# Kernel tuning notes

Measured on AMD Instinct MI355X. Metric: run time of the kernel, lower is better.

The kernel has to match this reference:

```python
import jax, jax.numpy as jnp
import numpy as np

C_IN, C_OUT = 256, 128

def setup_inputs() -> dict:
    key = jax.random.key(0)
    k1, k2, k3, k4, k5, k6 = jax.random.split(key, 6)
    B, H, W = 8, 64, 64
    p = jax.random.normal(k1, (B, C_IN, H, W), dtype=jnp.float32)
    b = jax.random.normal(k2, (B, C_IN, H, W), dtype=jnp.float32)
    # 1x1 conv weights (Conv2d with kernel 1 == pointwise matmul) + biases
    sq = 1.0 / np.sqrt(C_IN)
    Wq = jax.random.uniform(k3, (C_OUT, C_IN), jnp.float32, -sq, sq)
    bq = jax.random.uniform(k4, (C_OUT,), jnp.float32, -sq, sq)
    Wk = jax.random.uniform(k5, (C_OUT, C_IN), jnp.float32, -sq, sq)
    bk = jax.random.uniform(k6, (C_OUT,), jnp.float32, -sq, sq)
    return {"p": p, "b": b, "Wq": Wq, "bq": bq, "Wk": Wk, "bk": bk}

def reference(p, b, Wq, bq, Wk, bk):
    B, C, H, W = p.shape
    N = H * W
    # 1x1 convs -> flatten spatial dim to N
    q = jnp.einsum('bchw,oc->bhwo', p, Wq) + bq          # [B,H,W,Co]
    q = q.reshape(B, N, -1).astype(jnp.float32)           # [B,N,Co] (query permuted)
    k = jnp.einsum('bchw,oc->bohw', b, Wk) + bk[None, :, None, None]
    k = k.reshape(B, -1, N).astype(jnp.float32)           # [B,Co,N]
    energy = jnp.einsum('bnc,bcm->bnm', q, k)             # [B,N,N] unscaled
    attention = jax.nn.softmax(energy, axis=-1)           # softmax over keys
    value = b.reshape(B, C, N)                            # [B,C,N]
    out = jnp.einsum('bnm,bcm->bcn', attention, value)    # [B,C,N]
    return out.reshape(B, C, H, W)
```

## Files before the change

### kernel.cpp

```cpp
#include <hip/hip_runtime.h>
#include <hip/hip_bf16.h>
#include <math.h>


#define B_   8
#define CIN  256
#define COUT 128
#define NN   4096

typedef _Float16 half8  __attribute__((ext_vector_type(8)));
typedef short    short8 __attribute__((ext_vector_type(8)));
typedef float    f32x4  __attribute__((ext_vector_type(4)));

#define LOG2E 1.44269504088896340736f

__device__ __forceinline__ unsigned short f2h(float f) {
    union { _Float16 h; unsigned short u; } v; v.h = (_Float16)f;
    return v.u;
}
__device__ __forceinline__ unsigned int cvt_pk_bf16(float lo, float hi) {
    unsigned int r;
    asm("v_cvt_pk_bf16_f32 %0, %1, %2" : "=v"(r) : "v"(lo), "v"(hi));
    return r;
}
__device__ __forceinline__ unsigned int pkrtz(float lo, float hi) {
    typedef __fp16 fp16x2 __attribute__((ext_vector_type(2)));
    union { fp16x2 h; unsigned int u; } c;
    c.h = __builtin_amdgcn_cvt_pkrtz(lo, hi);
    return c.u;
}
__device__ __forceinline__ float dpp_xor1(float x) {
    union { float f; int i; } u; u.f = x;
    u.i = __builtin_amdgcn_mov_dpp(u.i, 0xB1, 0xF, 0xF, true);
    return u.f;
}
__device__ __forceinline__ void dma16(void* lds, const void* g) {
    __builtin_amdgcn_global_load_lds(
        (const __attribute__((address_space(1))) unsigned int*)g,
        (__attribute__((address_space(3))) unsigned int*)lds,
        16, 0, 0);
}

__global__ __launch_bounds__(256) void cvt_w(const float* __restrict__ Wq,
                                             const float* __restrict__ Wk,
                                             const float* __restrict__ bq,
                                             _Float16* __restrict__ Whq,
                                             _Float16* __restrict__ Whk,
                                             float* __restrict__ bqs) {
    const int bx = blockIdx.x, t = threadIdx.x;
    const int isK = (bx >= 32);
    const float* src = isK ? Wk : Wq;
    _Float16* dst = isK ? Whk : Whq;
    const float scale = isK ? 1.0f : LOG2E;
    const int idx = (bx & 31) * 256 + t;
    float4 v = ((const float4*)src)[idx];
    unsigned long long pk = (unsigned long long)f2h(v.x * scale)
                          | ((unsigned long long)f2h(v.y * scale) << 16)
                          | ((unsigned long long)f2h(v.z * scale) << 32)
                          | ((unsigned long long)f2h(v.w * scale) << 48);
    ((unsigned long long*)dst)[idx] = pk;
    if (bx == 0 && t < COUT) bqs[t] = bq[t] * LOG2E;
}

__global__ __launch_bounds__(256) void kv_prep(
        const float* __restrict__ Bv,
        const _Float16* __restrict__ Whk,
        const float* __restrict__ bk,
        _Float16* __restrict__ Ktt,
        unsigned short* __restrict__ Vb)
{
    __shared__ __align__(16) unsigned short T[64 * 136];
    const int bx = blockIdx.x;
    const int b  = bx >> 6, n0 = (bx & 63) << 6;
    const int t  = threadIdx.x;

    {
        const int cr = t >> 2;
        const int nch = (t & 3) << 4;
#pragma unroll
        for (int it = 0; it < 4; ++it) {
            const int c = it * 64 + cr;
            const float* src = Bv + ((size_t)(b * CIN + c) * NN + n0 + nch);
            unsigned int o2[8];
#pragma unroll
            for (int k = 0; k < 4; ++k) {
                float4 f = *(const float4*)(src + k * 4);
                o2[k * 2]     = cvt_pk_bf16(f.x, f.y);
                o2[k * 2 + 1] = cvt_pk_bf16(f.z, f.w);
            }
            unsigned short* dst = Vb + (size_t)(b * CIN + c) * NN + n0 + nch;
            *(int4*)dst = *(int4*)&o2[0];
            *(int4*)(dst + 8) = *(int4*)&o2[4];
        }
    }

    const int w = t >> 6, lane = t & 63, l15 = lane & 15, quad = lane >> 4, q8 = quad * 8;

    half8 a[8];
    {
        const float* Xa = Bv + ((size_t)(b * CIN + q8) * NN) + n0 + w * 16 + l15;
#pragma unroll
        for (int s = 0; s < 8; ++s) {
            const float* xs = Xa + (size_t)s * 32 * NN;
            float av[8];
#pragma unroll
            for (int j = 0; j < 8; ++j) av[j] = xs[(size_t)j * NN];
            union { half8 h; unsigned int u[4]; } af;
#pragma unroll
            for (int j = 0; j < 4; ++j) af.u[j] = pkrtz(av[2 * j], av[2 * j + 1]);
            a[s] = af.h;
        }
    }

    f32x4 D[8];
#pragma unroll
    for (int og = 0; og < 8; ++og) D[og] = (f32x4){0.f, 0.f, 0.f, 0.f};
    const _Float16* wbase = Whk + (size_t)l15 * CIN + q8;
#pragma unroll
    for (int s = 0; s < 8; ++s) {
        const _Float16* wp = wbase + s * 32;
#pragma unroll
        for (int og = 0; og < 8; ++og) {
            half8 wfv = *(const half8*)(wp + og * 16 * CIN);
            D[og] = __builtin_amdgcn_mfma_f32_16x16x32_f16(a[s], wfv, D[og], 0, 0, 0);
        }
    }

    const int nrow = w * 16 + quad * 4;
#pragma unroll
    for (int og = 0; og < 8; ++og) {
        const int o = og * 16 + l15;
        const float bo = bk[o];
        const int c = o >> 3, j = o & 7;
        const int sw = (c & 7) << 2;
#pragma unroll
        for (int r2 = 0; r2 < 4; ++r2) {
            const int n = nrow + r2;
            const int tl = n >> 5, m = n & 31;
            T[tl * 4096 + (c * 32 + ((m + sw) & 31)) * 8 + j] = f2h(D[og][r2] + bo);
        }
    }
    __syncthreads();
    _Float16* dstk = Ktt + ((size_t)(b * 128 + (n0 >> 5)) * 4096 + t * 32);
    const unsigned short* srck = T + t * 32;
#pragma unroll
    for (int k = 0; k < 4; ++k)
        ((int4*)dstk)[k] = ((const int4*)srck)[k];
}

__global__ __launch_bounds__(256, 3) void flash_kernel(const float* __restrict__ Pin,
                                                       const _Float16* __restrict__ Whq,
                                                       const float* __restrict__ bqs,
                                                       const _Float16* __restrict__ Ktt,
                                                       const unsigned short* __restrict__ V,
                                                       float* __restrict__ out) {
    __shared__ __align__(16) char SH[27136];
    _Float16*       K0sh = (_Float16*)(SH);
    _Float16*       K1sh = (_Float16*)(SH + 8192);
    unsigned short* P0sh = (unsigned short*)(SH + 16384);
    unsigned short* P1sh = (unsigned short*)(SH + 21504);
    float*          Lsh  = (float*)(SH + 26624);
    unsigned short* T    = (unsigned short*)SH;

    const int bx   = blockIdx.x;
    const int b    = bx >> 6;
    const int q0   = (bx & 63) << 6;
    const int t    = threadIdx.x;
    const int w    = t >> 6;
    const int lane = t & 63;
    const int l15  = lane & 15;
    const int quad = lane >> 4;
    const int q8   = quad * 8;

    const _Float16* Kb = Ktt + (size_t)b * 128 * 4096;
    const unsigned short* Vg = V + (size_t)b * CIN * NN;

    half8 Qf[4];
    {
        half8 a[8];
        const float* Xa = Pin + ((size_t)(b * CIN + q8) * NN) + q0 + w * 16 + l15;
#pragma unroll
        for (int s = 0; s < 8; ++s) {
            const float* xs = Xa + (size_t)s * 32 * NN;
            float av[8];
#pragma unroll
            for (int j = 0; j < 8; ++j) av[j] = xs[(size_t)j * NN];
            union { half8 h; unsigned int u[4]; } af;
#pragma unroll
            for (int j = 0; j < 4; ++j) af.u[j] = pkrtz(av[2 * j], av[2 * j + 1]);
            a[s] = af.h;
        }
        f32x4 D[8];
#pragma unroll
        for (int og = 0; og < 8; ++og) D[og] = (f32x4){0.f, 0.f, 0.f, 0.f};
        const _Float16* wbase = Whq + (size_t)l15 * CIN + q8;
#pragma unroll
        for (int s = 0; s < 8; ++s) {
            const _Float16* wp = wbase + s * 32;
#pragma unroll
            for (int og = 0; og < 8; ++og) {
                half8 wfv = *(const half8*)(wp + og * 16 * CIN);
                D[og] = __builtin_amdgcn_mfma_f32_16x16x32_f16(a[s], wfv, D[og], 0, 0, 0);
            }
        }
        const int nrow = w * 16 + quad * 4;
#pragma unroll
        for (int og = 0; og < 8; ++og) {
            const int o = og * 16 + l15;
            const float bo = bqs[o];
#pragma unroll
            for (int r2 = 0; r2 < 4; ++r2)
                T[(nrow + r2) * 136 + o] = f2h(D[og][r2] + bo);
        }
        __syncthreads();
#pragma unroll
        for (int s = 0; s < 4; ++s)
            Qf[s] = *(const half8*)&T[(w * 16 + l15) * 136 + s * 32 + q8];
        __syncthreads();
    }

    f32x4 O[16];
#pragma unroll
    for (int i = 0; i < 16; ++i) O[i] = (f32x4){0.f, 0.f, 0.f, 0.f};
    float lsum[4] = {0.f, 0.f, 0.f, 0.f};

    const unsigned short* Vlane = Vg + (size_t)(w * 64 + l15) * NN + q8;
    short8 VA[4], VB[4];

    auto issueK = [&](int kt, _Float16* Kd) {
        const _Float16* gk = Kb + (size_t)kt * 4096;
        dma16(Kd + (w * 2 + 0) * 512, gk + (w * 2 + 0) * 512 + lane * 8);
        dma16(Kd + (w * 2 + 1) * 512, gk + (w * 2 + 1) * 512 + lane * 8);
    };
    auto loadV = [&](int kt, short8* Vd) {
#pragma unroll
        for (int cj = 0; cj < 4; ++cj)
            Vd[cj] = *(const short8*)(Vlane + (size_t)cj * 16 * NN + kt * 32);
    };

    auto halfstep = [&](int kt, const _Float16* Kc, _Float16* Kn,
                        unsigned short* Pc, short8* Vcur) {
        if (kt + 1 < 128) issueK(kt + 1, Kn);

        f32x4 S0 = {0.f, 0.f, 0.f, 0.f}, S1 = {0.f, 0.f, 0.f, 0.f};
        __builtin_amdgcn_s_setprio(1);
#pragma unroll
        for (int s = 0; s < 4; ++s) {
            const int kc = 4 * s + quad;
            const int sw = (kc & 7) << 2;
            const int x0 = (l15 + sw) & 31;
            half8 kf0 = *(const half8*)(Kc + (kc * 32 + x0) * 8);
            half8 kf1 = *(const half8*)(Kc + (kc * 32 + (x0 ^ 16)) * 8);
            S0 = __builtin_amdgcn_mfma_f32_16x16x32_f16(Qf[s], kf0, S0, 0, 0, 0);
            S1 = __builtin_amdgcn_mfma_f32_16x16x32_f16(Qf[s], kf1, S1, 0, 0, 0);
        }
        __builtin_amdgcn_s_setprio(0);

        f32x4 E0, E1;
#pragma unroll
        for (int r = 0; r < 4; ++r) {
            E0[r] = exp2f(S0[r]);
            E1[r] = exp2f(S1[r]);
            lsum[r] += E0[r] + E1[r];
        }
        {
            f32x4 P0, P1;
#pragma unroll
            for (int r = 0; r < 4; ++r) { P0[r] = dpp_xor1(E0[r]); P1[r] = dpp_xor1(E1[r]); }
            const int odd = l15 & 1;
            unsigned short* wp0 = Pc + w * 640
                                + (((quad << 2) + (odd << 1)) * 40) + (l15 & ~1);
            unsigned int pk0 = cvt_pk_bf16(odd ? P0[2] : E0[0], odd ? E0[2] : P0[0]);
            unsigned int pk1 = cvt_pk_bf16(odd ? P0[3] : E0[1], odd ? E0[3] : P0[1]);
            unsigned int pk2 = cvt_pk_bf16(odd ? P1[2] : E1[0], odd ? E1[2] : P1[0]);
            unsigned int pk3 = cvt_pk_bf16(odd ? P1[3] : E1[1], odd ? E1[3] : P1[1]);
            *(unsigned int*)&wp0[0]  = pk0;
            *(unsigned int*)&wp0[40] = pk1;
            *(unsigned int*)&wp0[16] = pk2;
            *(unsigned int*)&wp0[56] = pk3;
        }

        __syncthreads();

        {
            short8 pf[4];
#pragma unroll
            for (int ni = 0; ni < 4; ++ni)
                pf[ni] = *(const short8*)(Pc + (ni * 16 + l15) * 40 + q8);
            __builtin_amdgcn_s_setprio(1);
#pragma unroll
            for (int cj = 0; cj < 4; ++cj) {
                short8 vf = Vcur[cj];
#pragma unroll
                for (int ni = 0; ni < 4; ++ni)
                    O[ni * 4 + cj] = __builtin_amdgcn_mfma_f32_16x16x32_bf16(pf[ni], vf, O[ni * 4 + cj], 0, 0, 0);
            }
            __builtin_amdgcn_s_setprio(0);
        }
        if (kt + 2 < 128) loadV(kt + 2, Vcur);
    };

    issueK(0, K0sh);
    loadV(0, VA);
    loadV(1, VB);
    __syncthreads();

#pragma unroll 1
    for (int kt = 0; kt < 128; kt += 2) {
        halfstep(kt,     K0sh, K1sh, P0sh, VA);
        halfstep(kt + 1, K1sh, K0sh, P1sh, VB);
    }

#pragma unroll
    for (int r = 0; r < 4; ++r) {
        float s = lsum[r];
        s += __shfl_xor(s, 1);
        s += __shfl_xor(s, 2);
        s += __shfl_xor(s, 4);
        s += __shfl_xor(s, 8);
        if (l15 == 0) Lsh[w * 16 + (quad << 2) + r] = s;
    }
    __syncthreads();
    float* ob = out + (size_t)b * CIN * NN + q0;
#pragma unroll
    for (int ni = 0; ni < 4; ++ni) {
        const f32x4 lv = *(const f32x4*)&Lsh[ni * 16 + (quad << 2)];
        f32x4 linv;
#pragma unroll
        for (int r = 0; r < 4; ++r) linv[r] = 1.0f / lv[r];
        const int nb = ni * 16 + (quad << 2);
#pragma unroll
        for (int cj = 0; cj < 4; ++cj) {
            const int c = w * 64 + cj * 16 + l15;
            f32x4 val = O[ni * 4 + cj];
#pragma unroll
            for (int r = 0; r < 4; ++r) val[r] *= linv[r];
            *(f32x4*)(ob + (size_t)c * NN + nb) = val;
        }
    }
}

extern "C" void kernel_launch(void* const* d_in, const int* in_sizes, int n_in,
                              void* d_out, int out_size, void* d_ws, size_t ws_size,
                              hipStream_t stream) {
    const float* p  = (const float*)d_in[0];
    const float* bv = (const float*)d_in[1];
    const float* Wq = (const float*)d_in[2];
    const float* bq = (const float*)d_in[3];
    const float* Wk = (const float*)d_in[4];
    const float* bk = (const float*)d_in[5];
    float* outp = (float*)d_out;

    char* ws = (char*)d_ws;
    const size_t szK = (size_t)B_ * NN * COUT * 2;
    const size_t szV = (size_t)B_ * NN * CIN * 2;
    const size_t szW = (size_t)COUT * CIN * 2;
    _Float16*       Ktt = (_Float16*)ws;
    unsigned short* Vb  = (unsigned short*)(ws + szK);
    _Float16*       Whq = (_Float16*)(ws + szK + szV);
    _Float16*       Whk = (_Float16*)(ws + szK + szV + szW);
    float*          bqs = (float*)(ws + szK + szV + 2 * szW);

    cvt_w<<<64, 256, 0, stream>>>(Wq, Wk, bq, Whq, Whk, bqs);
    kv_prep<<<512, 256, 0, stream>>>(bv, Whk, bk, Ktt, Vb);
    flash_kernel<<<512, 256, 0, stream>>>(p, Whq, bqs, Ktt, Vb, outp);
}
```

Baseline: 274.4 us.

## Fold weight conversion into consumers, split S accumulators, lower occupancy bound

Drops the separate weight-conversion kernel: kv_prep and flash_kernel now read fp32 weights directly and convert them to fp16 in registers, and the LOG2E scaling moves onto the query inputs and bias. This saves one launch, at the cost of extra weight load traffic and conversion work inside every block. The QK^T MFMA chain is split into two independent accumulators so consecutive MFMAs no longer depend on each other, and the halfstep body is factored into S and PV lambdas. The flash kernel's launch bound is relaxed from 3 to 2 blocks per CU, which gives more registers per thread but may lower occupancy.

Result: slower. 302.2 us (+10.1%).

```diff
diff --git a/kernel.cpp b/kernel.cpp
--- a/kernel.cpp
+++ b/kernel.cpp
@@ -29,6 +29,16 @@
     c.h = __builtin_amdgcn_cvt_pkrtz(lo, hi);
     return c.u;
 }
+__device__ __forceinline__ half8 ld_w8(const float* p) {
+    float4 w0 = *(const float4*)(p);
+    float4 w1 = *(const float4*)(p + 4);
+    union { half8 h; unsigned int u[4]; } c;
+    c.u[0] = pkrtz(w0.x, w0.y);
+    c.u[1] = pkrtz(w0.z, w0.w);
+    c.u[2] = pkrtz(w1.x, w1.y);
+    c.u[3] = pkrtz(w1.z, w1.w);
+    return c.h;
+}
 __device__ __forceinline__ float dpp_xor1(float x) {
     union { float f; int i; } u; u.f = x;
     u.i = __builtin_amdgcn_mov_dpp(u.i, 0xB1, 0xF, 0xF, true);
@@ -41,30 +51,9 @@
         16, 0, 0);
 }
 
-__global__ __launch_bounds__(256) void cvt_w(const float* __restrict__ Wq,
-                                             const float* __restrict__ Wk,
-                                             const float* __restrict__ bq,
-                                             _Float16* __restrict__ Whq,
-                                             _Float16* __restrict__ Whk,
-                                             float* __restrict__ bqs) {
-    const int bx = blockIdx.x, t = threadIdx.x;
-    const int isK = (bx >= 32);
-    const float* src = isK ? Wk : Wq;
-    _Float16* dst = isK ? Whk : Whq;
-    const float scale = isK ? 1.0f : LOG2E;
-    const int idx = (bx & 31) * 256 + t;
-    float4 v = ((const float4*)src)[idx];
-    unsigned long long pk = (unsigned long long)f2h(v.x * scale)
-                          | ((unsigned long long)f2h(v.y * scale) << 16)
-                          | ((unsigned long long)f2h(v.z * scale) << 32)
-                          | ((unsigned long long)f2h(v.w * scale) << 48);
-    ((unsigned long long*)dst)[idx] = pk;
-    if (bx == 0 && t < COUT) bqs[t] = bq[t] * LOG2E;
-}
-
 __global__ __launch_bounds__(256) void kv_prep(
         const float* __restrict__ Bv,
-        const _Float16* __restrict__ Whk,
+        const float* __restrict__ Wk,
         const float* __restrict__ bk,
         _Float16* __restrict__ Ktt,
         unsigned short* __restrict__ Vb)
@@ -115,13 +104,13 @@
     f32x4 D[8];
 #pragma unroll
     for (int og = 0; og < 8; ++og) D[og] = (f32x4){0.f, 0.f, 0.f, 0.f};
-    const _Float16* wbase = Whk + (size_t)l15 * CIN + q8;
+    const float* wbase = Wk + (size_t)l15 * CIN + q8;
 #pragma unroll
     for (int s = 0; s < 8; ++s) {
-        const _Float16* wp = wbase + s * 32;
+        const float* wp = wbase + s * 32;
 #pragma unroll
         for (int og = 0; og < 8; ++og) {
-            half8 wfv = *(const half8*)(wp + og * 16 * CIN);
+            half8 wfv = ld_w8(wp + (size_t)og * 16 * CIN);
             D[og] = __builtin_amdgcn_mfma_f32_16x16x32_f16(a[s], wfv, D[og], 0, 0, 0);
         }
     }
@@ -148,9 +137,9 @@
         ((int4*)dstk)[k] = ((const int4*)srck)[k];
 }
 
-__global__ __launch_bounds__(256, 3) void flash_kernel(const float* __restrict__ Pin,
-                                                       const _Float16* __restrict__ Whq,
-                                                       const float* __restrict__ bqs,
+__global__ __launch_bounds__(256, 2) void flash_kernel(const float* __restrict__ Pin,
+                                                       const float* __restrict__ Wq,
+                                                       const float* __restrict__ bq,
                                                        const _Float16* __restrict__ Ktt,
                                                        const unsigned short* __restrict__ V,
                                                        float* __restrict__ out) {
@@ -184,7 +173,7 @@
             const float* xs = Xa + (size_t)s * 32 * NN;
             float av[8];
 #pragma unroll
-            for (int j = 0; j < 8; ++j) av[j] = xs[(size_t)j * NN];
+            for (int j = 0; j < 8; ++j) av[j] = xs[(size_t)j * NN] * LOG2E;
             union { half8 h; unsigned int u[4]; } af;
 #pragma unroll
             for (int j = 0; j < 4; ++j) af.u[j] = pkrtz(av[2 * j], av[2 * j + 1]);
@@ -193,13 +182,13 @@
         f32x4 D[8];
 #pragma unroll
         for (int og = 0; og < 8; ++og) D[og] = (f32x4){0.f, 0.f, 0.f, 0.f};
-        const _Float16* wbase = Whq + (size_t)l15 * CIN + q8;
+        const float* wbase = Wq + (size_t)l15 * CIN + q8;
 #pragma unroll
         for (int s = 0; s < 8; ++s) {
-            const _Float16* wp = wbase + s * 32;
+            const float* wp = wbase + s * 32;
 #pragma unroll
             for (int og = 0; og < 8; ++og) {
-                half8 wfv = *(const half8*)(wp + og * 16 * CIN);
+                half8 wfv = ld_w8(wp + (size_t)og * 16 * CIN);
                 D[og] = __builtin_amdgcn_mfma_f32_16x16x32_f16(a[s], wfv, D[og], 0, 0, 0);
             }
         }
@@ -207,7 +196,7 @@
 #pragma unroll
         for (int og = 0; og < 8; ++og) {
             const int o = og * 16 + l15;
-            const float bo = bqs[o];
+            const float bo = bq[o] * LOG2E;
 #pragma unroll
             for (int r2 = 0; r2 < 4; ++r2)
                 T[(nrow + r2) * 136 + o] = f2h(D[og][r2] + bo);
@@ -238,11 +227,10 @@
             Vd[cj] = *(const short8*)(Vlane + (size_t)cj * 16 * NN + kt * 32);
     };
 
-    auto halfstep = [&](int kt, const _Float16* Kc, _Float16* Kn,
-                        unsigned short* Pc, short8* Vcur) {
-        if (kt + 1 < 128) issueK(kt + 1, Kn);
-
-        f32x4 S0 = {0.f, 0.f, 0.f, 0.f}, S1 = {0.f, 0.f, 0.f, 0.f};
+    auto Sphase = [&](int kt, unsigned short* Pc) {
+        const _Float16* Kc = (kt & 1) ? K1sh : K0sh;
+        f32x4 S0a = {0.f, 0.f, 0.f, 0.f}, S0b = {0.f, 0.f, 0.f, 0.f};
+        f32x4 S1a = {0.f, 0.f, 0.f, 0.f}, S1b = {0.f, 0.f, 0.f, 0.f};
         __builtin_amdgcn_s_setprio(1);
 #pragma unroll
         for (int s = 0; s < 4; ++s) {
@@ -251,52 +239,60 @@
             const int x0 = (l15 + sw) & 31;
             half8 kf0 = *(const half8*)(Kc + (kc * 32 + x0) * 8);
             half8 kf1 = *(const half8*)(Kc + (kc * 32 + (x0 ^ 16)) * 8);
-            S0 = __builtin_amdgcn_mfma_f32_16x16x32_f16(Qf[s], kf0, S0, 0, 0, 0);
-            S1 = __builtin_amdgcn_mfma_f32_16x16x32_f16(Qf[s], kf1, S1, 0, 0, 0);
+            if (s & 1) {
+                S0b = __builtin_amdgcn_mfma_f32_16x16x32_f16(Qf[s], kf0, S0b, 0, 0, 0);
+                S1b = __builtin_amdgcn_mfma_f32_16x16x32_f16(Qf[s], kf1, S1b, 0, 0, 0);
+            } else {
+                S0a = __builtin_amdgcn_mfma_f32_16x16x32_f16(Qf[s], kf0, S0a, 0, 0, 0);
+                S1a = __builtin_amdgcn_mfma_f32_16x16x32_f16(Qf[s], kf1, S1a, 0, 0, 0);
+            }
         }
         __builtin_amdgcn_s_setprio(0);
 
         f32x4 E0, E1;
 #pragma unroll
         for (int r = 0; r < 4; ++r) {
-            E0[r] = exp2f(S0[r]);
-            E1[r] = exp2f(S1[r]);
+            E0[r] = exp2f(S0a[r] + S0b[r]);
+            E1[r] = exp2f(S1a[r] + S1b[r]);
             lsum[r] += E0[r] + E1[r];
         }
-        {
-            f32x4 P0, P1;
-#pragma unroll
-            for (int r = 0; r < 4; ++r) { P0[r] = dpp_xor1(E0[r]); P1[r] = dpp_xor1(E1[r]); }
-            const int odd = l15 & 1;
-            unsigned short* wp0 = Pc + w * 640
-                                + (((quad << 2) + (odd << 1)) * 40) + (l15 & ~1);
-            unsigned int pk0 = cvt_pk_bf16(odd ? P0[2] : E0[0], odd ? E0[2] : P0[0]);
-            unsigned int pk1 = cvt_pk_bf16(odd ? P0[3] : E0[1], odd ? E0[3] : P0[1]);
-            unsigned int pk2 = cvt_pk_bf16(odd ? P1[2] : E1[0], odd ? E1[2] : P1[0]);
-            unsigned int pk3 = cvt_pk_bf16(odd ? P1[3] : E1[1], odd ? E1[3] : P1[1]);
-            *(unsigned int*)&wp0[0]  = pk0;
-            *(unsigned int*)&wp0[40] = pk1;
-            *(unsigned int*)&wp0[16] = pk2;
-            *(unsigned int*)&wp0[56] = pk3;
-        }
-
+        f32x4 P0, P1;
+#pragma unroll
+        for (int r = 0; r < 4; ++r) { P0[r] = dpp_xor1(E0[r]); P1[r] = dpp_xor1(E1[r]); }
+        const int odd = l15 & 1;
+        unsigned short* wp0 = Pc + w * 640
+                            + (((quad << 2) + (odd << 1)) * 40) + (l15 & ~1);
+        unsigned int pk0 = cvt_pk_bf16(odd ? P0[2] : E0[0], odd ? E0[2] : P0[0]);
+        unsigned int pk1 = cvt_pk_bf16(odd ? P0[3] : E0[1], odd ? E0[3] : P0[1]);
+        unsigned int pk2 = cvt_pk_bf16(odd ? P1[2] : E1[0], odd ? E1[2] : P1[0]);
+        unsigned int pk3 = cvt_pk_bf16(odd ? P1[3] : E1[1], odd ? E1[3] : P1[1]);
+        *(unsigned int*)&wp0[0]  = pk0;
+        *(unsigned int*)&wp0[40] = pk1;
+        *(unsigned int*)&wp0[16] = pk2;
+        *(unsigned int*)&wp0[56] = pk3;
+    };
+
+    auto PVphase = [&](const unsigned short* Pc, const short8* Vc) {
+        short8 pf[4];
+#pragma unroll
+        for (int ni = 0; ni < 4; ++ni)
+            pf[ni] = *(const short8*)(Pc + (ni * 16 + l15) * 40 + q8);
+        __builtin_amdgcn_s_setprio(1);
+#pragma unroll
+        for (int cj = 0; cj < 4; ++cj) {
+            short8 vf = Vc[cj];
+#pragma unroll
+            for (int ni = 0; ni < 4; ++ni)
+                O[ni * 4 + cj] = __builtin_amdgcn_mfma_f32_16x16x32_bf16(pf[ni], vf, O[ni * 4 + cj], 0, 0, 0);
+        }
+        __builtin_amdgcn_s_setprio(0);
+    };
+
+    auto halfstep = [&](int kt, _Float16* Kn, unsigned short* Pc, short8* Vcur) {
+        if (kt + 1 < 128) issueK(kt + 1, Kn);
+        Sphase(kt, Pc);
         __syncthreads();
-
-        {
-            short8 pf[4];
-#pragma unroll
-            for (int ni = 0; ni < 4; ++ni)
-                pf[ni] = *(const short8*)(Pc + (ni * 16 + l15) * 40 + q8);
-            __builtin_amdgcn_s_setprio(1);
-#pragma unroll
-            for (int cj = 0; cj < 4; ++cj) {
-                short8 vf = Vcur[cj];
-#pragma unroll
-                for (int ni = 0; ni < 4; ++ni)
-                    O[ni * 4 + cj] = __builtin_amdgcn_mfma_f32_16x16x32_bf16(pf[ni], vf, O[ni * 4 + cj], 0, 0, 0);
-            }
-            __builtin_amdgcn_s_setprio(0);
-        }
+        PVphase(Pc, Vcur);
         if (kt + 2 < 128) loadV(kt + 2, Vcur);
     };
 
@@ -307,8 +303,8 @@
 
 #pragma unroll 1
     for (int kt = 0; kt < 128; kt += 2) {
-        halfstep(kt,     K0sh, K1sh, P0sh, VA);
-        halfstep(kt + 1, K1sh, K0sh, P1sh, VB);
+        halfstep(kt,     K1sh, P0sh, VA);
+        halfstep(kt + 1, K0sh, P1sh, VB);
     }
 
 #pragma unroll
@@ -353,15 +349,9 @@
 
     char* ws = (char*)d_ws;
     const size_t szK = (size_t)B_ * NN * COUT * 2;
-    const size_t szV = (size_t)B_ * NN * CIN * 2;
-    const size_t szW = (size_t)COUT * CIN * 2;
     _Float16*       Ktt = (_Float16*)ws;
     unsigned short* Vb  = (unsigned short*)(ws + szK);
-    _Float16*       Whq = (_Float16*)(ws + szK + szV);
-    _Float16*       Whk = (_Float16*)(ws + szK + szV + szW);
-    float*          bqs = (float*)(ws + szK + szV + 2 * szW);
-
-    cvt_w<<<64, 256, 0, stream>>>(Wq, Wk, bq, Whq, Whk, bqs);
-    kv_prep<<<512, 256, 0, stream>>>(bv, Whk, bk, Ktt, Vb);
-    flash_kernel<<<512, 256, 0, stream>>>(p, Whq, bqs, Ktt, Vb, outp);
-}
+
+    kv_prep<<<512, 256, 0, stream>>>(bv, Wk, bk, Ktt, Vb);
+    flash_kernel<<<512, 256, 0, stream>>>(p, Wq, bq, Ktt, Vb, outp);
+}
```
